# Optimization experiments

Hardware: AMD Instinct MI355X
Metric: run time of the kernel (lower is better)

The kernel has to match this reference:

```python
import jax, jax.numpy as jnp
import numpy as np

N_NODES = 100000
N_EDGES = 3200000
D_IN = 256
D_OUT = 256


def setup_inputs() -> dict:
    key = jax.random.key(0)
    k1, k2, k3, k4, k5 = jax.random.split(key, 5)
    x = jax.random.normal(k1, (N_NODES, D_IN), dtype=jnp.float32)
    weight = jax.random.normal(k2, (D_IN, D_OUT), dtype=jnp.float32)
    edge_rows = jax.random.randint(k3, (N_EDGES,), 0, N_NODES, dtype=jnp.int32)
    edge_cols = jax.random.randint(k4, (N_EDGES,), 0, N_NODES, dtype=jnp.int32)
    edge_vals = jax.random.uniform(k5, (N_EDGES,), dtype=jnp.float32)
    return {"x": x, "weight": weight, "edge_rows": edge_rows,
            "edge_cols": edge_cols, "edge_vals": edge_vals}


def reference(x, weight, edge_rows, edge_cols, edge_vals):
    # GraphConvolution forward (eval mode, dense features, no bias):
    #   xw  = x @ W                      [N, D_OUT]
    #   out = relu(A_sparse @ xw)        A given as COO edge list
    xw = x @ weight  # [N, D_OUT]
    msgs = edge_vals[:, None] * xw[edge_cols]  # gather source features, scale
    agg = jax.ops.segment_sum(msgs, edge_rows, num_segments=N_NODES)
    return jax.nn.relu(agg)
```

## Files before the change

### kernel.cpp

```cpp
#include <hip/hip_runtime.h>
#include <hip/hip_bf16.h>

#define N_NODES 100000
#define N_EDGES 3200000
#define D 256
#define RSH 7
#define RPB 128
#define NB ((N_NODES + RPB - 1) / RPB)
#define FILL_CH 8192
#define NBLK_E ((N_EDGES + FILL_CH - 1) / FILL_CH)

typedef __attribute__((ext_vector_type(8))) short short8;
typedef __attribute__((ext_vector_type(4))) float floatx4;

__device__ __forceinline__ unsigned short f32_to_bf16_rne(float f) {
    unsigned int u = __float_as_uint(f);
    u += 0x7FFFu + ((u >> 16) & 1u);
    return (unsigned short)(u >> 16);
}
__device__ __forceinline__ float bf16_bits_to_f32(unsigned short b) {
    return __uint_as_float(((unsigned int)b) << 16);
}
__device__ __forceinline__ float blo(unsigned int x) { return __uint_as_float(x << 16); }
__device__ __forceinline__ float bhi(unsigned int x) { return __uint_as_float(x & 0xFFFF0000u); }

__global__ __launch_bounds__(256) void convert_w_k(const float* __restrict__ w,
                                                   unsigned short* __restrict__ wsw) {
    int t = blockIdx.x * 256 + threadIdx.x;
    int j     = t & 7;
    int lane  = (t >> 3) & 63;
    int kstep = (t >> 9) & 7;
    int ntile = t >> 12;
    int k = kstep * 32 + (lane >> 4) * 8 + j;
    int n = ntile * 16 + (lane & 15);
    wsw[t] = f32_to_bf16_rne(w[k * D + n]);
}

__global__ __launch_bounds__(512) void gemm_xw_k(const float* __restrict__ x,
                                                 const unsigned short* __restrict__ wsw,
                                                 unsigned short* __restrict__ xwb) {
    __shared__ uint4 wlds[8192];
    const int tid = threadIdx.x;
#pragma unroll
    for (int i = 0; i < 16; ++i) {
        int idx = i * 512 + tid;
        wlds[idx] = ((const uint4*)wsw)[idx];
    }
    __syncthreads();

    const int lane = tid & 63;
    const int wave = tid >> 6;
    const int q    = lane >> 4;
    const int ml   = lane & 15;
    const long rowBase = (long)blockIdx.x * 128 + wave * 16;
    long arow = rowBase + ml;
    if (arow >= N_NODES) arow = 0;
    const float* xr = x + arow * (long)D;

    floatx4 acc[16];
#pragma unroll
    for (int i = 0; i < 16; ++i) acc[i] = (floatx4){0.f, 0.f, 0.f, 0.f};

    const short8* wfrag = (const short8*)wlds;

#pragma unroll
    for (int ks = 0; ks < 8; ++ks) {
        const float4 a0 = *(const float4*)(xr + ks * 32 + q * 8);
        const float4 a1 = *(const float4*)(xr + ks * 32 + q * 8 + 4);
        short8 af;
        af[0] = (short)f32_to_bf16_rne(a0.x);
        af[1] = (short)f32_to_bf16_rne(a0.y);
        af[2] = (short)f32_to_bf16_rne(a0.z);
        af[3] = (short)f32_to_bf16_rne(a0.w);
        af[4] = (short)f32_to_bf16_rne(a1.x);
        af[5] = (short)f32_to_bf16_rne(a1.y);
        af[6] = (short)f32_to_bf16_rne(a1.z);
        af[7] = (short)f32_to_bf16_rne(a1.w);
#pragma unroll
        for (int nt = 0; nt < 16; ++nt) {
            acc[nt] = __builtin_amdgcn_mfma_f32_16x16x32_bf16(
                af, wfrag[(nt * 8 + ks) * 64 + lane], acc[nt], 0, 0, 0);
        }
    }

#pragma unroll
    for (int nt = 0; nt < 16; ++nt) {
#pragma unroll
        for (int r = 0; r < 4; ++r) {
            long orow = rowBase + q * 4 + r;
            if (orow < N_NODES)
                xwb[orow * (long)D + nt * 16 + ml] = f32_to_bf16_rne(acc[nt][r]);
        }
    }
}

__global__ __launch_bounds__(256) void bhist_k(const int* __restrict__ erow,
                                               int* __restrict__ counts) {
    __shared__ int h[NB];
    const int tid = threadIdx.x;
    for (int i = tid; i < NB; i += 256) h[i] = 0;
    __syncthreads();
    const int s = blockIdx.x * FILL_CH;
    const int e = min(s + FILL_CH, N_EDGES);
    for (int i = s + tid; i < e; i += 256) atomicAdd(&h[erow[i] >> RSH], 1);
    __syncthreads();
    for (int i = tid; i < NB; i += 256)
        if (h[i] > 0) atomicAdd(&counts[i], h[i]);
}

__global__ __launch_bounds__(1024) void bscan_k(const int* __restrict__ counts,
                                                int* __restrict__ bbase,
                                                int* __restrict__ bcursor) {
    __shared__ int sc[1024];
    const int t = threadIdx.x;
    int v = (t < NB) ? counts[t] : 0;
    sc[t] = v;
    __syncthreads();
    for (int o = 1; o < 1024; o <<= 1) {
        int add = (t >= o) ? sc[t - o] : 0;
        __syncthreads();
        sc[t] += add;
        __syncthreads();
    }
    int excl = sc[t] - v;
    if (t < NB) { bbase[t] = excl; bcursor[t] = excl; }
    if (t == NB - 1) bbase[NB] = sc[t];
}

__global__ __launch_bounds__(256) void binfill_k(const int* __restrict__ erow,
                                                 const int* __restrict__ ecol,
                                                 const float* __restrict__ eval,
                                                 int* __restrict__ bcursor,
                                                 unsigned long long* __restrict__ recs) {
    __shared__ int h[NB];
    __shared__ int lcur[NB];
    const int tid = threadIdx.x;
    for (int i = tid; i < NB; i += 256) h[i] = 0;
    __syncthreads();
    const int s = blockIdx.x * FILL_CH;
    const int e = min(s + FILL_CH, N_EDGES);
    for (int i = s + tid; i < e; i += 256) atomicAdd(&h[erow[i] >> RSH], 1);
    __syncthreads();
    for (int i = tid; i < NB; i += 256) {
        int cnt = h[i];
        lcur[i] = (cnt > 0) ? atomicAdd(&bcursor[i], cnt) : 0;
    }
    __syncthreads();
    for (int i = s + tid; i < e; i += 256) {
        int r = erow[i];
        int b = r >> RSH;
        int pos = atomicAdd(&lcur[b], 1);
        unsigned long long rec =
            ((unsigned long long)(r & (RPB - 1)) << 33) |
            ((unsigned long long)f32_to_bf16_rne(eval[i]) << 17) |
            (unsigned int)ecol[i];
        recs[pos] = rec;
    }
}

__global__ __launch_bounds__(256) void bsort_k(const int* __restrict__ bbase,
                                               const unsigned long long* __restrict__ recs,
                                               int* __restrict__ offsets,
                                               unsigned int* __restrict__ cs,
                                               unsigned short* __restrict__ vs) {
    __shared__ int hist[RPB];
    __shared__ int cur[RPB];
    __shared__ int sc[RPB];
    const int t = threadIdx.x;
    const int b = blockIdx.x;
    const int base = bbase[b];
    const int endp = bbase[b + 1];

    if (t < RPB) hist[t] = 0;
    __syncthreads();
    for (int i = base + t; i < endp; i += 256)
        atomicAdd(&hist[(int)(recs[i] >> 33)], 1);
    __syncthreads();

    if (t < RPB) sc[t] = hist[t];
    __syncthreads();
    for (int o = 1; o < RPB; o <<= 1) {
        int add = (t >= o && t < RPB) ? sc[t - o] : 0;
        __syncthreads();
        if (t < RPB) sc[t] += add;
        __syncthreads();
    }
    if (t < RPB) {
        int excl = sc[t] - hist[t];
        cur[t] = excl;
        int r = (b << RSH) + t;
        if (r <= N_NODES) offsets[r] = base + excl;
    }
    __syncthreads();

    for (int i = base + t; i < endp; i += 256) {
        unsigned long long rec = recs[i];
        int rl = (int)(rec >> 33);
        int pos = base + atomicAdd(&cur[rl], 1);
        cs[pos] = (unsigned int)(rec & 0x1FFFFu);
        vs[pos] = (unsigned short)((rec >> 17) & 0xFFFFu);
    }
}

__global__ __launch_bounds__(256) void aggregate_k(const unsigned short* __restrict__ xwb,
                                                   const int* __restrict__ offsets,
                                                   const unsigned int* __restrict__ cs,
                                                   const unsigned short* __restrict__ vs,
                                                   float* __restrict__ out) {
    const int wave = threadIdx.x >> 6;
    const int lane = threadIdx.x & 63;
    const int r = blockIdx.x * 4 + wave;
    if (r >= N_NODES) return;

    const int start = offsets[r];
    const int end   = offsets[r + 1];
    const int half  = lane >> 5;
    const int hl    = lane & 31;

    float acc[8];
#pragma unroll
    for (int k = 0; k < 8; ++k) acc[k] = 0.f;

#pragma unroll 1
    for (int jb = start; jb < end; jb += 64) {
        int j = jb + lane;
        unsigned int c = 0;
        float v = 0.f;
        if (j < end) {
            c = cs[j];
            v = bf16_bits_to_f32(vs[j]);
        }
        const int cnt = min(64, end - jb);
        const int pairs = (cnt + 1) >> 1;
        const int hp = cnt >> 1;
        int t = 0;

#define FMA8(qv, bv)                                                           \
        acc[0] += bv * blo(qv.x); acc[1] += bv * bhi(qv.x);                    \
        acc[2] += bv * blo(qv.y); acc[3] += bv * bhi(qv.y);                    \
        acc[4] += bv * blo(qv.z); acc[5] += bv * bhi(qv.z);                    \
        acc[6] += bv * blo(qv.w); acc[7] += bv * bhi(qv.w);
#define SLOTF(s, qv, bv)                                                       \
        {                                                                      \
            int src = 2 * (t + (s)) + half;                                    \
            unsigned int bc = (unsigned int)__shfl((int)c, src);               \
            bv = __shfl(v, src);                                               \
            qv = ((const uint4*)(xwb + (size_t)bc * D))[hl];                   \
        }

#pragma unroll 1
        for (; t + 8 <= hp; t += 8) {
            uint4 q0, q1, q2, q3, q4, q5, q6, q7;
            float b0, b1, b2, b3, b4, b5, b6, b7;
            SLOTF(0, q0, b0) SLOTF(1, q1, b1) SLOTF(2, q2, b2) SLOTF(3, q3, b3)
            SLOTF(4, q4, b4) SLOTF(5, q5, b5) SLOTF(6, q6, b6) SLOTF(7, q7, b7)
            FMA8(q0, b0) FMA8(q1, b1) FMA8(q2, b2) FMA8(q3, b3)
            FMA8(q4, b4) FMA8(q5, b5) FMA8(q6, b6) FMA8(q7, b7)
        }
        if (t + 4 <= hp) {
            uint4 q0, q1, q2, q3;
            float b0, b1, b2, b3;
            SLOTF(0, q0, b0) SLOTF(1, q1, b1) SLOTF(2, q2, b2) SLOTF(3, q3, b3)
            FMA8(q0, b0) FMA8(q1, b1) FMA8(q2, b2) FMA8(q3, b3)
            t += 4;
        }
#undef SLOTF

#pragma unroll 1
        for (; t < pairs; ++t) {
            int src = 2 * t + half;
            int srcc = min(src, cnt - 1);
            unsigned int bc = (unsigned int)__shfl((int)c, srcc);
            float bb = __shfl(v, srcc);
            float bv = (src < cnt) ? bb : 0.f;
            uint4 q = ((const uint4*)(xwb + (size_t)bc * D))[hl];
            FMA8(q, bv)
        }
#undef FMA8
    }

#pragma unroll
    for (int k = 0; k < 8; ++k) acc[k] += __shfl_xor(acc[k], 32);

    const int s = lane >> 1;
    const int par = lane & 1;
    float4 o;
    {
        float a0 = __shfl(acc[0], s), b0 = __shfl(acc[4], s);
        float a1 = __shfl(acc[1], s), b1 = __shfl(acc[5], s);
        float a2 = __shfl(acc[2], s), b2 = __shfl(acc[6], s);
        float a3 = __shfl(acc[3], s), b3 = __shfl(acc[7], s);
        o.x = par ? b0 : a0;
        o.y = par ? b1 : a1;
        o.z = par ? b2 : a2;
        o.w = par ? b3 : a3;
    }
    o.x = fmaxf(o.x, 0.f);
    o.y = fmaxf(o.y, 0.f);
    o.z = fmaxf(o.z, 0.f);
    o.w = fmaxf(o.w, 0.f);
    ((float4*)(out + (size_t)r * D))[lane] = o;
}

extern "C" void kernel_launch(void* const* d_in, const int* in_sizes, int n_in,
                              void* d_out, int out_size, void* d_ws, size_t ws_size,
                              hipStream_t stream) {
    const float* x    = (const float*)d_in[0];
    const float* w    = (const float*)d_in[1];
    const int*   erow = (const int*)d_in[2];
    const int*   ecol = (const int*)d_in[3];
    const float* eval = (const float*)d_in[4];
    float* out = (float*)d_out;

    char* p = (char*)d_ws;
    auto align = [](size_t v) { return (v + 255) & ~(size_t)255; };

    unsigned short* xwb = (unsigned short*)p;
    p += align((size_t)N_NODES * D * sizeof(unsigned short));
    unsigned short* wsw = (unsigned short*)p;
    p += align((size_t)D * D * sizeof(unsigned short));
    int* bcounts = (int*)p;  p += align((size_t)NB * sizeof(int));
    int* bbase   = (int*)p;  p += align((size_t)(NB + 1) * sizeof(int));
    int* bcursor = (int*)p;  p += align((size_t)NB * sizeof(int));
    unsigned long long* recs = (unsigned long long*)p;
    p += align((size_t)N_EDGES * sizeof(unsigned long long));
    unsigned int*   cs = (unsigned int*)p;    p += align((size_t)N_EDGES * 4);
    unsigned short* vs = (unsigned short*)p;  p += align((size_t)N_EDGES * 2);
    int* offsets = (int*)p;  p += align((size_t)(N_NODES + 1) * sizeof(int));

    convert_w_k<<<(D * D) / 256, 256, 0, stream>>>(w, wsw);
    gemm_xw_k<<<(N_NODES + 127) / 128, 512, 0, stream>>>(x, wsw, xwb);
    hipMemsetAsync(bcounts, 0, (size_t)NB * sizeof(int), stream);
    bhist_k<<<NBLK_E, 256, 0, stream>>>(erow, bcounts);
    bscan_k<<<1, 1024, 0, stream>>>(bcounts, bbase, bcursor);
    binfill_k<<<NBLK_E, 256, 0, stream>>>(erow, ecol, eval, bcursor, recs);
    bsort_k<<<NB, 256, 0, stream>>>(bbase, recs, offsets, cs, vs);
    aggregate_k<<<(N_NODES + 3) / 4, 256, 0, stream>>>(xwb, offsets, cs, vs, out);
}
```

Baseline: 587.7 us.

## Replace two-level bucket sort with direct per-row counting sort into CSR

Replaces the bucketed histogram, bin-fill and per-bucket sort passes with a single global per-row histogram, a two-kernel parallel prefix scan, and a direct atomic scatter into CSR column and value arrays. This drops the intermediate 64-bit record buffer and one full pass over the edges. In exchange it relies on global atomics on 100k counters, where the old code used shared-memory atomics, and the scatter writes are less coalesced.

```diff
diff --git a/kernel.cpp b/kernel.cpp
--- a/kernel.cpp
+++ b/kernel.cpp
@@ -4,11 +4,8 @@
 #define N_NODES 100000
 #define N_EDGES 3200000
 #define D 256
-#define RSH 7
-#define RPB 128
-#define NB ((N_NODES + RPB - 1) / RPB)
-#define FILL_CH 8192
-#define NBLK_E ((N_EDGES + FILL_CH - 1) / FILL_CH)
+#define SCAN_CH 2048
+#define NBLK_S ((N_NODES + 1 + SCAN_CH - 1) / SCAN_CH)
 
 typedef __attribute__((ext_vector_type(8))) short short8;
 typedef __attribute__((ext_vector_type(4))) float floatx4;
@@ -94,111 +91,86 @@
     }
 }
 
-__global__ __launch_bounds__(256) void bhist_k(const int* __restrict__ erow,
-                                               int* __restrict__ counts) {
-    __shared__ int h[NB];
-    const int tid = threadIdx.x;
-    for (int i = tid; i < NB; i += 256) h[i] = 0;
+__global__ __launch_bounds__(256) void rhist_k(const int* __restrict__ erow,
+                                               int* __restrict__ rcnt) {
+    int i = blockIdx.x * 256 + threadIdx.x;
+    const int stride = gridDim.x * 256;
+    for (; i < N_EDGES; i += stride) atomicAdd(&rcnt[erow[i]], 1);
+}
+
+__global__ __launch_bounds__(1024) void scanA_k(const int* __restrict__ rcnt,
+                                                int* __restrict__ offsets,
+                                                int* __restrict__ bsums) {
+    const int t = threadIdx.x;
+    const int g = blockIdx.x * SCAN_CH + 2 * t;
+    int v0 = (g     < N_NODES + 1) ? rcnt[g]     : 0;
+    int v1 = (g + 1 < N_NODES + 1) ? rcnt[g + 1] : 0;
+    int s = v0 + v1;
+
+    const int lane = t & 63;
+    const int wv   = t >> 6;
+    int x = s;
+#pragma unroll
+    for (int d = 1; d < 64; d <<= 1) {
+        int u = __shfl_up(x, d);
+        if (lane >= d) x += u;
+    }
+    __shared__ int wsum[16];
+    if (lane == 63) wsum[wv] = x;
     __syncthreads();
-    const int s = blockIdx.x * FILL_CH;
-    const int e = min(s + FILL_CH, N_EDGES);
-    for (int i = s + tid; i < e; i += 256) atomicAdd(&h[erow[i] >> RSH], 1);
+    if (wv == 0) {
+        int y = (lane < 16) ? wsum[lane] : 0;
+#pragma unroll
+        for (int d = 1; d < 16; d <<= 1) {
+            int u = __shfl_up(y, d);
+            if (lane >= d) y += u;
+        }
+        if (lane < 16) wsum[lane] = y;
+    }
     __syncthreads();
-    for (int i = tid; i < NB; i += 256)
-        if (h[i] > 0) atomicAdd(&counts[i], h[i]);
-}
-
-__global__ __launch_bounds__(1024) void bscan_k(const int* __restrict__ counts,
-                                                int* __restrict__ bbase,
-                                                int* __restrict__ bcursor) {
-    __shared__ int sc[1024];
-    const int t = threadIdx.x;
-    int v = (t < NB) ? counts[t] : 0;
-    sc[t] = v;
+    int waveoff = (wv > 0) ? wsum[wv - 1] : 0;
+    int sincl = x + waveoff;
+    int excl0 = sincl - s;
+    if (g     < N_NODES + 1) offsets[g]     = excl0;
+    if (g + 1 < N_NODES + 1) offsets[g + 1] = excl0 + v0;
+    if (t == 1023) bsums[blockIdx.x] = sincl;
+}
+
+__global__ __launch_bounds__(1024) void scanB_k(const int* __restrict__ bsums,
+                                                int* __restrict__ offsets,
+                                                int* __restrict__ cursor) {
+    __shared__ int soff;
+    if (threadIdx.x == 0) {
+        int a = 0;
+        for (int i = 0; i < blockIdx.x; ++i) a += bsums[i];
+        soff = a;
+    }
     __syncthreads();
-    for (int o = 1; o < 1024; o <<= 1) {
-        int add = (t >= o) ? sc[t - o] : 0;
-        __syncthreads();
-        sc[t] += add;
-        __syncthreads();
-    }
-    int excl = sc[t] - v;
-    if (t < NB) { bbase[t] = excl; bcursor[t] = excl; }
-    if (t == NB - 1) bbase[NB] = sc[t];
-}
-
-__global__ __launch_bounds__(256) void binfill_k(const int* __restrict__ erow,
+    const int g = blockIdx.x * SCAN_CH + 2 * threadIdx.x;
+#pragma unroll
+    for (int k = 0; k < 2; ++k) {
+        int gg = g + k;
+        if (gg < N_NODES + 1) {
+            int o = offsets[gg] + soff;
+            offsets[gg] = o;
+            if (gg < N_NODES) cursor[gg] = o;
+        }
+    }
+}
+
+__global__ __launch_bounds__(256) void scatter_k(const int* __restrict__ erow,
                                                  const int* __restrict__ ecol,
                                                  const float* __restrict__ eval,
-                                                 int* __restrict__ bcursor,
-                                                 unsigned long long* __restrict__ recs) {
-    __shared__ int h[NB];
-    __shared__ int lcur[NB];
-    const int tid = threadIdx.x;
-    for (int i = tid; i < NB; i += 256) h[i] = 0;
-    __syncthreads();
-    const int s = blockIdx.x * FILL_CH;
-    const int e = min(s + FILL_CH, N_EDGES);
-    for (int i = s + tid; i < e; i += 256) atomicAdd(&h[erow[i] >> RSH], 1);
-    __syncthreads();
-    for (int i = tid; i < NB; i += 256) {
-        int cnt = h[i];
-        lcur[i] = (cnt > 0) ? atomicAdd(&bcursor[i], cnt) : 0;
-    }
-    __syncthreads();
-    for (int i = s + tid; i < e; i += 256) {
+                                                 int* __restrict__ cursor,
+                                                 unsigned int* __restrict__ cs,
+                                                 unsigned short* __restrict__ vs) {
+    int i = blockIdx.x * 256 + threadIdx.x;
+    const int stride = gridDim.x * 256;
+    for (; i < N_EDGES; i += stride) {
         int r = erow[i];
-        int b = r >> RSH;
-        int pos = atomicAdd(&lcur[b], 1);
-        unsigned long long rec =
-            ((unsigned long long)(r & (RPB - 1)) << 33) |
-            ((unsigned long long)f32_to_bf16_rne(eval[i]) << 17) |
-            (unsigned int)ecol[i];
-        recs[pos] = rec;
-    }
-}
-
-__global__ __launch_bounds__(256) void bsort_k(const int* __restrict__ bbase,
-                                               const unsigned long long* __restrict__ recs,
-                                               int* __restrict__ offsets,
-                                               unsigned int* __restrict__ cs,
-                                               unsigned short* __restrict__ vs) {
-    __shared__ int hist[RPB];
-    __shared__ int cur[RPB];
-    __shared__ int sc[RPB];
-    const int t = threadIdx.x;
-    const int b = blockIdx.x;
-    const int base = bbase[b];
-    const int endp = bbase[b + 1];
-
-    if (t < RPB) hist[t] = 0;
-    __syncthreads();
-    for (int i = base + t; i < endp; i += 256)
-        atomicAdd(&hist[(int)(recs[i] >> 33)], 1);
-    __syncthreads();
-
-    if (t < RPB) sc[t] = hist[t];
-    __syncthreads();
-    for (int o = 1; o < RPB; o <<= 1) {
-        int add = (t >= o && t < RPB) ? sc[t - o] : 0;
-        __syncthreads();
-        if (t < RPB) sc[t] += add;
-        __syncthreads();
-    }
-    if (t < RPB) {
-        int excl = sc[t] - hist[t];
-        cur[t] = excl;
-        int r = (b << RSH) + t;
-        if (r <= N_NODES) offsets[r] = base + excl;
-    }
-    __syncthreads();
-
-    for (int i = base + t; i < endp; i += 256) {
-        unsigned long long rec = recs[i];
-        int rl = (int)(rec >> 33);
-        int pos = base + atomicAdd(&cur[rl], 1);
-        cs[pos] = (unsigned int)(rec & 0x1FFFFu);
-        vs[pos] = (unsigned short)((rec >> 17) & 0xFFFFu);
+        int pos = atomicAdd(&cursor[r], 1);
+        cs[pos] = (unsigned int)ecol[i];
+        vs[pos] = f32_to_bf16_rne(eval[i]);
     }
 }
 
@@ -319,21 +291,19 @@
     p += align((size_t)N_NODES * D * sizeof(unsigned short));
     unsigned short* wsw = (unsigned short*)p;
     p += align((size_t)D * D * sizeof(unsigned short));
-    int* bcounts = (int*)p;  p += align((size_t)NB * sizeof(int));
-    int* bbase   = (int*)p;  p += align((size_t)(NB + 1) * sizeof(int));
-    int* bcursor = (int*)p;  p += align((size_t)NB * sizeof(int));
-    unsigned long long* recs = (unsigned long long*)p;
-    p += align((size_t)N_EDGES * sizeof(unsigned long long));
+    int* rcnt    = (int*)p;  p += align((size_t)(N_NODES + 1) * sizeof(int));
+    int* offsets = (int*)p;  p += align((size_t)(N_NODES + 1) * sizeof(int));
+    int* cursor  = (int*)p;  p += align((size_t)N_NODES * sizeof(int));
+    int* bsums   = (int*)p;  p += align((size_t)64 * sizeof(int));
     unsigned int*   cs = (unsigned int*)p;    p += align((size_t)N_EDGES * 4);
     unsigned short* vs = (unsigned short*)p;  p += align((size_t)N_EDGES * 2);
-    int* offsets = (int*)p;  p += align((size_t)(N_NODES + 1) * sizeof(int));
 
     convert_w_k<<<(D * D) / 256, 256, 0, stream>>>(w, wsw);
     gemm_xw_k<<<(N_NODES + 127) / 128, 512, 0, stream>>>(x, wsw, xwb);
-    hipMemsetAsync(bcounts, 0, (size_t)NB * sizeof(int), stream);
-    bhist_k<<<NBLK_E, 256, 0, stream>>>(erow, bcounts);
-    bscan_k<<<1, 1024, 0, stream>>>(bcounts, bbase, bcursor);
-    binfill_k<<<NBLK_E, 256, 0, stream>>>(erow, ecol, eval, bcursor, recs);
-    bsort_k<<<NB, 256, 0, stream>>>(bbase, recs, offsets, cs, vs);
+    hipMemsetAsync(rcnt, 0, (size_t)(N_NODES + 1) * sizeof(int), stream);
+    rhist_k<<<2048, 256, 0, stream>>>(erow, rcnt);
+    scanA_k<<<NBLK_S, 1024, 0, stream>>>(rcnt, offsets, bsums);
+    scanB_k<<<NBLK_S, 1024, 0, stream>>>(bsums, offsets, cursor);
+    scatter_k<<<2048, 256, 0, stream>>>(erow, ecol, eval, cursor, cs, vs);
     aggregate_k<<<(N_NODES + 3) / 4, 256, 0, stream>>>(xwb, offsets, cs, vs, out);
 }
```

Result: slower. 812.8 us (+38.3%).

## Make edge binning deterministic with per-block offsets and LDS-staged coalesced writes

Applied to the files above, without the earlier changes.

Replaces global-atomic bin cursors with a per-block histogram matrix, a column prefix scan and a total scan, so every block knows its exact output offsets. The bin-fill kernel now stages records in LDS sorted by bin and writes each bin's run out contiguously instead of scattering 8-byte records. Bins grow to 256 rows and the sort kernel caches each bin's records in LDS, with a global-memory fallback for large bins. The aim is less scattered global write traffic and fewer global atomics, at the cost of extra scan kernels and heavy LDS use (about 115KB and 72KB per block), which limits occupancy.

```diff
diff --git a/kernel.cpp b/kernel.cpp
--- a/kernel.cpp
+++ b/kernel.cpp
@@ -4,11 +4,13 @@
 #define N_NODES 100000
 #define N_EDGES 3200000
 #define D 256
-#define RSH 7
-#define RPB 128
-#define NB ((N_NODES + RPB - 1) / RPB)
-#define FILL_CH 8192
-#define NBLK_E ((N_EDGES + FILL_CH - 1) / FILL_CH)
+
+#define RSH2 8
+#define RPB2 256
+#define NB2 ((N_NODES + RPB2 - 1) / RPB2)
+#define FILL_CH 14336
+#define NBLK_F ((N_EDGES + FILL_CH - 1) / FILL_CH)
+#define MAX_BREC 9216
 
 typedef __attribute__((ext_vector_type(8))) short short8;
 typedef __attribute__((ext_vector_type(4))) float floatx4;
@@ -94,108 +96,205 @@
     }
 }
 
-__global__ __launch_bounds__(256) void bhist_k(const int* __restrict__ erow,
-                                               int* __restrict__ counts) {
-    __shared__ int h[NB];
+__global__ __launch_bounds__(256) void hist2_k(const int* __restrict__ erow,
+                                               int* __restrict__ C) {
+    __shared__ int h[NB2];
     const int tid = threadIdx.x;
-    for (int i = tid; i < NB; i += 256) h[i] = 0;
+    for (int i = tid; i < NB2; i += 256) h[i] = 0;
     __syncthreads();
     const int s = blockIdx.x * FILL_CH;
     const int e = min(s + FILL_CH, N_EDGES);
-    for (int i = s + tid; i < e; i += 256) atomicAdd(&h[erow[i] >> RSH], 1);
-    __syncthreads();
-    for (int i = tid; i < NB; i += 256)
-        if (h[i] > 0) atomicAdd(&counts[i], h[i]);
-}
-
-__global__ __launch_bounds__(1024) void bscan_k(const int* __restrict__ counts,
-                                                int* __restrict__ bbase,
-                                                int* __restrict__ bcursor) {
-    __shared__ int sc[1024];
+    for (int i = s + tid; i < e; i += 256) atomicAdd(&h[erow[i] >> RSH2], 1);
+    __syncthreads();
+    for (int b = tid; b < NB2; b += 256) C[b * NBLK_F + blockIdx.x] = h[b];
+}
+
+__global__ __launch_bounds__(256) void colprefix_k(int* __restrict__ C,
+                                                   int* __restrict__ tot) {
+    const int wave_id = blockIdx.x * 4 + (threadIdx.x >> 6);
+    const int lane = threadIdx.x & 63;
+    if (wave_id >= NB2) return;
+    int* row = C + wave_id * NBLK_F;
+    int run = 0;
+#pragma unroll
+    for (int ch = 0; ch < NBLK_F; ch += 64) {
+        int idx = ch + lane;
+        int v = (idx < NBLK_F) ? row[idx] : 0;
+        int x = v;
+#pragma unroll
+        for (int d = 1; d < 64; d <<= 1) {
+            int u = __shfl_up(x, d);
+            if (lane >= d) x += u;
+        }
+        int excl = x - v;
+        if (idx < NBLK_F) row[idx] = run + excl;
+        run += __shfl(x, 63);
+    }
+    if (lane == 0) tot[wave_id] = run;
+}
+
+__global__ __launch_bounds__(512) void totscan_k(const int* __restrict__ tot,
+                                                 int* __restrict__ bbase) {
+    __shared__ int wsum[8];
     const int t = threadIdx.x;
-    int v = (t < NB) ? counts[t] : 0;
-    sc[t] = v;
-    __syncthreads();
-    for (int o = 1; o < 1024; o <<= 1) {
-        int add = (t >= o) ? sc[t - o] : 0;
+    const int lane = t & 63;
+    const int wv = t >> 6;
+    int v = (t < NB2) ? tot[t] : 0;
+    int x = v;
+#pragma unroll
+    for (int d = 1; d < 64; d <<= 1) {
+        int u = __shfl_up(x, d);
+        if (lane >= d) x += u;
+    }
+    if (lane == 63) wsum[wv] = x;
+    __syncthreads();
+    if (wv == 0) {
+        int y = (lane < 8) ? wsum[lane] : 0;
+#pragma unroll
+        for (int d = 1; d < 8; d <<= 1) {
+            int u = __shfl_up(y, d);
+            if (lane >= d) y += u;
+        }
+        if (lane < 8) wsum[lane] = y;
+    }
+    __syncthreads();
+    int excl = x - v + ((wv > 0) ? wsum[wv - 1] : 0);
+    if (t < NB2) bbase[t] = excl;
+    if (t == NB2 - 1) bbase[NB2] = excl + v;
+}
+
+__global__ __launch_bounds__(256) void binfill2_k(const int* __restrict__ erow,
+                                                  const int* __restrict__ ecol,
+                                                  const float* __restrict__ eval,
+                                                  const int* __restrict__ C,
+                                                  const int* __restrict__ bbase,
+                                                  unsigned long long* __restrict__ recs) {
+    __shared__ unsigned long long lrec[FILL_CH];
+    __shared__ int h[NB2];
+    __shared__ int cur[NB2];
+    __shared__ int gb[NB2];
+    __shared__ int wsum[4];
+    const int tid = threadIdx.x;
+    const int blk = blockIdx.x;
+    const int s = blk * FILL_CH;
+    const int e = min(s + FILL_CH, N_EDGES);
+
+    for (int i = tid; i < NB2; i += 256) h[i] = 0;
+    __syncthreads();
+
+    for (int i = s + tid; i < e; i += 256) atomicAdd(&h[erow[i] >> RSH2], 1);
+    __syncthreads();
+
+    {
+        const int b0 = 2 * tid, b1 = 2 * tid + 1;
+        int v0 = (b0 < NB2) ? h[b0] : 0;
+        int v1 = (b1 < NB2) ? h[b1] : 0;
+        int sv = v0 + v1;
+        const int lane = tid & 63;
+        const int wv = tid >> 6;
+        int x = sv;
+#pragma unroll
+        for (int d = 1; d < 64; d <<= 1) {
+            int u = __shfl_up(x, d);
+            if (lane >= d) x += u;
+        }
+        if (lane == 63) wsum[wv] = x;
         __syncthreads();
-        sc[t] += add;
+        if (wv == 0) {
+            int y = (lane < 4) ? wsum[lane] : 0;
+#pragma unroll
+            for (int d = 1; d < 4; d <<= 1) {
+                int u = __shfl_up(y, d);
+                if (lane >= d) y += u;
+            }
+            if (lane < 4) wsum[lane] = y;
+        }
         __syncthreads();
-    }
-    int excl = sc[t] - v;
-    if (t < NB) { bbase[t] = excl; bcursor[t] = excl; }
-    if (t == NB - 1) bbase[NB] = sc[t];
-}
-
-__global__ __launch_bounds__(256) void binfill_k(const int* __restrict__ erow,
-                                                 const int* __restrict__ ecol,
-                                                 const float* __restrict__ eval,
-                                                 int* __restrict__ bcursor,
-                                                 unsigned long long* __restrict__ recs) {
-    __shared__ int h[NB];
-    __shared__ int lcur[NB];
-    const int tid = threadIdx.x;
-    for (int i = tid; i < NB; i += 256) h[i] = 0;
-    __syncthreads();
-    const int s = blockIdx.x * FILL_CH;
-    const int e = min(s + FILL_CH, N_EDGES);
-    for (int i = s + tid; i < e; i += 256) atomicAdd(&h[erow[i] >> RSH], 1);
-    __syncthreads();
-    for (int i = tid; i < NB; i += 256) {
-        int cnt = h[i];
-        lcur[i] = (cnt > 0) ? atomicAdd(&bcursor[i], cnt) : 0;
-    }
-    __syncthreads();
+        int excl = x - sv + ((wv > 0) ? wsum[wv - 1] : 0);
+        if (b0 < NB2) cur[b0] = excl;
+        if (b1 < NB2) cur[b1] = excl + v0;
+        for (int b = tid; b < NB2; b += 256) gb[b] = bbase[b] + C[b * NBLK_F + blk];
+    }
+    __syncthreads();
+
     for (int i = s + tid; i < e; i += 256) {
         int r = erow[i];
-        int b = r >> RSH;
-        int pos = atomicAdd(&lcur[b], 1);
+        int b = r >> RSH2;
         unsigned long long rec =
-            ((unsigned long long)(r & (RPB - 1)) << 33) |
+            ((unsigned long long)(r & (RPB2 - 1)) << 33) |
             ((unsigned long long)f32_to_bf16_rne(eval[i]) << 17) |
             (unsigned int)ecol[i];
-        recs[pos] = rec;
-    }
-}
-
-__global__ __launch_bounds__(256) void bsort_k(const int* __restrict__ bbase,
-                                               const unsigned long long* __restrict__ recs,
-                                               int* __restrict__ offsets,
-                                               unsigned int* __restrict__ cs,
-                                               unsigned short* __restrict__ vs) {
-    __shared__ int hist[RPB];
-    __shared__ int cur[RPB];
-    __shared__ int sc[RPB];
+        int pos = atomicAdd(&cur[b], 1);
+        lrec[pos] = rec;
+    }
+    __syncthreads();
+
+    const int lane = tid & 63;
+    const int wv = tid >> 6;
+    for (int b = wv; b < NB2; b += 4) {
+        int len = h[b];
+        int start = cur[b] - len;
+        int gdst = gb[b];
+        for (int o = lane; o < len; o += 64) recs[gdst + o] = lrec[start + o];
+    }
+}
+
+__global__ __launch_bounds__(256) void bsort2_k(const int* __restrict__ bbase,
+                                                const unsigned long long* __restrict__ recs,
+                                                int* __restrict__ offsets,
+                                                unsigned int* __restrict__ cs,
+                                                unsigned short* __restrict__ vs) {
+    __shared__ unsigned long long lrec[MAX_BREC];
+    __shared__ int hist[RPB2];
+    __shared__ int cur[RPB2];
+    __shared__ int wsum[4];
     const int t = threadIdx.x;
     const int b = blockIdx.x;
     const int base = bbase[b];
-    const int endp = bbase[b + 1];
-
-    if (t < RPB) hist[t] = 0;
-    __syncthreads();
-    for (int i = base + t; i < endp; i += 256)
-        atomicAdd(&hist[(int)(recs[i] >> 33)], 1);
-    __syncthreads();
-
-    if (t < RPB) sc[t] = hist[t];
-    __syncthreads();
-    for (int o = 1; o < RPB; o <<= 1) {
-        int add = (t >= o && t < RPB) ? sc[t - o] : 0;
+    const int nfull = bbase[b + 1] - base;
+    const int n = min(nfull, MAX_BREC);
+
+    for (int i = t; i < n; i += 256) lrec[i] = recs[base + i];
+    hist[t] = 0;
+    __syncthreads();
+    for (int i = t; i < nfull; i += 256) {
+        unsigned long long rec = (i < n) ? lrec[i] : recs[base + i];
+        atomicAdd(&hist[(int)((rec >> 33) & 255u)], 1);
+    }
+    __syncthreads();
+
+    {
+        int v = hist[t];
+        const int lane = t & 63;
+        const int wv = t >> 6;
+        int x = v;
+#pragma unroll
+        for (int d = 1; d < 64; d <<= 1) {
+            int u = __shfl_up(x, d);
+            if (lane >= d) x += u;
+        }
+        if (lane == 63) wsum[wv] = x;
         __syncthreads();
-        if (t < RPB) sc[t] += add;
+        if (wv == 0) {
+            int y = (lane < 4) ? wsum[lane] : 0;
+#pragma unroll
+            for (int d = 1; d < 4; d <<= 1) {
+                int u = __shfl_up(y, d);
+                if (lane >= d) y += u;
+            }
+            if (lane < 4) wsum[lane] = y;
+        }
         __syncthreads();
-    }
-    if (t < RPB) {
-        int excl = sc[t] - hist[t];
+        int excl = x - v + ((wv > 0) ? wsum[wv - 1] : 0);
         cur[t] = excl;
-        int r = (b << RSH) + t;
+        int r = (b << RSH2) + t;
         if (r <= N_NODES) offsets[r] = base + excl;
     }
     __syncthreads();
 
-    for (int i = base + t; i < endp; i += 256) {
-        unsigned long long rec = recs[i];
-        int rl = (int)(rec >> 33);
+    for (int i = t; i < nfull; i += 256) {
+        unsigned long long rec = (i < n) ? lrec[i] : recs[base + i];
+        int rl = (int)((rec >> 33) & 255u);
         int pos = base + atomicAdd(&cur[rl], 1);
         cs[pos] = (unsigned int)(rec & 0x1FFFFu);
         vs[pos] = (unsigned short)((rec >> 17) & 0xFFFFu);
@@ -319,9 +418,9 @@
     p += align((size_t)N_NODES * D * sizeof(unsigned short));
     unsigned short* wsw = (unsigned short*)p;
     p += align((size_t)D * D * sizeof(unsigned short));
-    int* bcounts = (int*)p;  p += align((size_t)NB * sizeof(int));
-    int* bbase   = (int*)p;  p += align((size_t)(NB + 1) * sizeof(int));
-    int* bcursor = (int*)p;  p += align((size_t)NB * sizeof(int));
+    int* C     = (int*)p;  p += align((size_t)NB2 * NBLK_F * sizeof(int));
+    int* tot   = (int*)p;  p += align((size_t)NB2 * sizeof(int));
+    int* bbase = (int*)p;  p += align((size_t)(NB2 + 1) * sizeof(int));
     unsigned long long* recs = (unsigned long long*)p;
     p += align((size_t)N_EDGES * sizeof(unsigned long long));
     unsigned int*   cs = (unsigned int*)p;    p += align((size_t)N_EDGES * 4);
@@ -330,10 +429,10 @@
 
     convert_w_k<<<(D * D) / 256, 256, 0, stream>>>(w, wsw);
     gemm_xw_k<<<(N_NODES + 127) / 128, 512, 0, stream>>>(x, wsw, xwb);
-    hipMemsetAsync(bcounts, 0, (size_t)NB * sizeof(int), stream);
-    bhist_k<<<NBLK_E, 256, 0, stream>>>(erow, bcounts);
-    bscan_k<<<1, 1024, 0, stream>>>(bcounts, bbase, bcursor);
-    binfill_k<<<NBLK_E, 256, 0, stream>>>(erow, ecol, eval, bcursor, recs);
-    bsort_k<<<NB, 256, 0, stream>>>(bbase, recs, offsets, cs, vs);
+    hist2_k<<<NBLK_F, 256, 0, stream>>>(erow, C);
+    colprefix_k<<<(NB2 + 3) / 4, 256, 0, stream>>>(C, tot);
+    totscan_k<<<1, 512, 0, stream>>>(tot, bbase);
+    binfill2_k<<<NBLK_F, 256, 0, stream>>>(erow, ecol, eval, C, bbase, recs);
+    bsort2_k<<<NB2, 256, 0, stream>>>(bbase, recs, offsets, cs, vs);
     aggregate_k<<<(N_NODES + 3) / 4, 256, 0, stream>>>(xwb, offsets, cs, vs, out);
 }
```

After: 564.8 us. 3.9% less time.
